# Optimization experiments

Measured on AMD Instinct MI355X. Metric: run time of the kernel, lower is better.

Reference implementation:

```python
import jax, jax.numpy as jnp
import numpy as np

B, T, C, H = 2, 2048, 1024, 16
D = C // H  # head_dim = 64

def setup_inputs() -> dict:
    key = jax.random.key(0)
    k0, k1, k2, k3, k4 = jax.random.split(key, 5)
    s = 1.0 / np.sqrt(C)
    return {
        "x": jax.random.normal(k0, (B, T, C), dtype=jnp.float32),
        "w_qkv": jax.random.uniform(k1, (C, 3 * C), jnp.float32, -s, s),
        "b_qkv": jax.random.uniform(k2, (3 * C,), jnp.float32, -s, s),
        "w_proj": jax.random.uniform(k3, (C, C), jnp.float32, -s, s),
        "b_proj": jax.random.uniform(k4, (C,), jnp.float32, -s, s),
    }

def reference(x, w_qkv, b_qkv, w_proj, b_proj):
    Bx, Tx, Cx = x.shape
    qkv = x @ w_qkv + b_qkv                      # [B,T,3C]
    q, k, v = jnp.split(qkv, 3, axis=-1)
    # [B,T,C] -> [B,H,T,D]
    def heads(t):
        return t.reshape(Bx, Tx, H, D).transpose(0, 2, 1, 3)
    q, k, v = heads(q), heads(k), heads(v)
    att = jnp.einsum('bhqd,bhkd->bhqk', q, k) / np.sqrt(D).astype(np.float32)
    causal = jnp.tril(jnp.ones((Tx, Tx), dtype=bool))
    att = jnp.where(causal, att, -jnp.inf)
    att = jax.nn.softmax(att, axis=-1)
    y = jnp.einsum('bhqk,bhkd->bhqd', att, v)    # [B,H,T,D]
    y = y.transpose(0, 2, 1, 3).reshape(Bx, Tx, Cx)
    return y @ w_proj + b_proj
```

## Files before the change

kernel.cpp:

```cpp
#include <hip/hip_runtime.h>

typedef short bf16x8 __attribute__((ext_vector_type(8)));
typedef float f32x4 __attribute__((ext_vector_type(4)));
typedef unsigned short u16;
typedef unsigned short u16x8 __attribute__((ext_vector_type(8)));
typedef unsigned short u16x4 __attribute__((ext_vector_type(4), may_alias));
typedef float f32x4_a __attribute__((ext_vector_type(4), may_alias));

__device__ __forceinline__ u16 f2bf(float f) {
    union { float f; unsigned u; } v; v.f = f;
    unsigned r = v.u + 0x7fffu + ((v.u >> 16) & 1u);
    return (u16)(r >> 16);
}
__device__ __forceinline__ u16 f2bf_rhu(float f) {
    union { float f; unsigned u; } v; v.f = f;
    return (u16)((v.u + 0x8000u) >> 16);
}

__device__ __forceinline__ void gld_lds16(const void* g, void* l) {
    __builtin_amdgcn_global_load_lds(
        (const __attribute__((address_space(1))) void*)g,
        (__attribute__((address_space(3))) void*)l, 16, 0, 0);
}

__global__ __launch_bounds__(256) void prep_kernel(
    const float* __restrict__ x, u16* __restrict__ xb,
    const float* __restrict__ w_qkv, u16* __restrict__ wqkvT,
    const float* __restrict__ w_proj, u16* __restrict__ wprojT) {
    __shared__ float tile[32][33];
    const int b = blockIdx.x, tid = threadIdx.x;
    if (b < 2048) {
        const int i = b * 256 + tid;
        float4 a = ((const float4*)x)[i * 2];
        float4 c = ((const float4*)x)[i * 2 + 1];
        u16x8 h;
        h[0] = f2bf(a.x); h[1] = f2bf(a.y); h[2] = f2bf(a.z); h[3] = f2bf(a.w);
        h[4] = f2bf(c.x); h[5] = f2bf(c.y); h[6] = f2bf(c.z); h[7] = f2bf(c.w);
        *(u16x8*)(xb + (size_t)i * 8) = h;
        return;
    }
    const float* in; u16* out; int N, bx;
    if (b < 5120) { bx = b - 2048; in = w_qkv; out = wqkvT; N = 3072; }
    else          { bx = b - 5120; in = w_proj; out = wprojT; N = 1024; }
    const int nblk = N / 32;
    const int n0 = (bx % nblk) * 32, k0 = (bx / nblk) * 32;
    const int tx = tid & 31, ty = tid >> 5;
#pragma unroll
    for (int i = 0; i < 32; i += 8)
        tile[ty + i][tx] = in[(size_t)(k0 + ty + i) * N + n0 + tx];
    __syncthreads();
#pragma unroll
    for (int i = 0; i < 32; i += 8)
        out[(size_t)(n0 + ty + i) * 1024 + k0 + tx] = f2bf(tile[tx][ty + i]);
}

#define QSCALE 0.180336880f

template <int OUTMODE, int BN>
__global__ __launch_bounds__(256) void gemm_m97(
    const u16* __restrict__ A, const u16* __restrict__ Bt,
    const float* __restrict__ bias, float* __restrict__ Cf,
    u16* __restrict__ Qo, u16* __restrict__ Ko, u16* __restrict__ Vt,
    int M, int N, int K) {
    constexpr int NF = BN / 32;
    __shared__ __align__(16) u16 lA[128 * 64];
    __shared__ __align__(16) u16 lB[BN * 64];

    const int tid = threadIdx.x;
    const int lane = tid & 63, wid = tid >> 6;
    const int wr = wid >> 1, wc = wid & 1;
    const int fr = lane & 15, fq = lane >> 4;
    const int m0 = blockIdx.y * 128, n0 = blockIdx.x * BN;

    const int gsrc = (lane & 7) ^ (lane >> 3);
    const u16* gA0 = A + (size_t)(m0 + (tid >> 3)) * K + gsrc * 8;
    const u16* gB0 = Bt + (size_t)(n0 + (tid >> 3)) * K + gsrc * 8;
    u16* lAw = lA + wid * 512;
    u16* lBw = lB + wid * 512;

    const int r7 = fr & 7;
    const int gk[2] = { ((0 + fq) ^ r7) * 8, ((4 + fq) ^ r7) * 8 };

    f32x4 acc[4][NF];
#pragma unroll
    for (int m = 0; m < 4; m++)
#pragma unroll
        for (int n = 0; n < NF; n++)
#pragma unroll
            for (int r = 0; r < 4; r++) acc[m][n][r] = 0.f;

    for (int k0 = 0; k0 < K; k0 += 64) {
        __syncthreads();
#pragma unroll
        for (int c = 0; c < 4; c++)
            gld_lds16(gA0 + (size_t)(c * 32) * K + k0, lAw + c * 2048);
#pragma unroll
        for (int c = 0; c < BN / 32; c++)
            gld_lds16(gB0 + (size_t)(c * 32) * K + k0, lBw + c * 2048);
        __syncthreads();

#pragma unroll
        for (int kf = 0; kf < 2; kf++) {
            bf16x8 a[4], b[NF];
#pragma unroll
            for (int m = 0; m < 4; m++)
                a[m] = *(const bf16x8*)&lA[(wr * 64 + m * 16 + fr) * 64 + gk[kf]];
#pragma unroll
            for (int n = 0; n < NF; n++)
                b[n] = *(const bf16x8*)&lB[(wc * (BN / 2) + n * 16 + fr) * 64 + gk[kf]];
#pragma unroll
            for (int m = 0; m < 4; m++)
#pragma unroll
                for (int n = 0; n < NF; n++)
                    acc[m][n] = __builtin_amdgcn_mfma_f32_16x16x32_bf16(a[m], b[n], acc[m][n], 0, 0, 0);
        }
    }

#pragma unroll
    for (int m = 0; m < 4; m++) {
#pragma unroll
        for (int n = 0; n < NF; n++) {
            const int row0 = m0 + wr * 64 + m * 16 + fq * 4;
            const int col = n0 + wc * (BN / 2) + n * 16 + fr;
            float v4[4];
#pragma unroll
            for (int r = 0; r < 4; r++) v4[r] = acc[m][n][r] + bias[col];
            if (OUTMODE == 0) {
                const int bb = row0 >> 11, t0 = row0 & 2047;
                const int sec = col >> 10, cc = col & 1023;
                const int h = cc >> 6, d = cc & 63;
                if (sec == 0) {
#pragma unroll
                    for (int r = 0; r < 4; r++)
                        Qo[(((size_t)(bb * 16 + h) * 2048 + t0 + r) << 6) + d] = f2bf(v4[r] * QSCALE);
                } else if (sec == 1) {
#pragma unroll
                    for (int r = 0; r < 4; r++)
                        Ko[(((size_t)(bb * 16 + h) * 2048 + t0 + r) << 6) + d] = f2bf(v4[r]);
                } else {
                    ushort4 p;
                    p.x = f2bf(v4[0]); p.y = f2bf(v4[1]); p.z = f2bf(v4[2]); p.w = f2bf(v4[3]);
                    *(ushort4*)&Vt[(((size_t)(bb * 16 + h) * 64 + d) << 11) + t0] = p;
                }
            } else {
#pragma unroll
                for (int r = 0; r < 4; r++)
                    Cf[(size_t)(row0 + r) * N + col] = v4[r];
            }
        }
    }
}

__global__ __launch_bounds__(256, 4) void attn_kernel(const u16* __restrict__ Q,
                                                      const u16* __restrict__ Kg,
                                                      const u16* __restrict__ Vt,
                                                      u16* __restrict__ O) {
    __shared__ __align__(16) u16 lK[2][64 * 64];
    __shared__ __align__(16) u16 lV[2][64 * 64];
    __shared__ __align__(16) u16 lP[4][32 * 32];

    const int tid = threadIdx.x;
    const int lane = tid & 63, wid = tid >> 6;
    const int fr = lane & 15, fq = lane >> 4;
    const int kw = wid >> 1, qw = wid & 1;
    const int bh = blockIdx.x & 31;
    const int qi = 31 - (blockIdx.x >> 5);
    const int qb0 = qi * 64;
    const size_t base = (size_t)bh * (2048 * 64);
    const u16* Qp = Q + base;
    const u16* Kp = Kg + base;
    const u16* Vp = Vt + base;

    const int q0w = qb0 + qw * 32;
    bf16x8 qa[2][2];
#pragma unroll
    for (int qg = 0; qg < 2; qg++)
#pragma unroll
        for (int kf = 0; kf < 2; kf++)
            qa[qg][kf] = *(const bf16x8*)&Qp[(size_t)(q0w + qg * 16 + fr) * 64 + kf * 32 + fq * 8];
    asm volatile("s_waitcnt vmcnt(0)" ::: "memory");

    bf16x8 vones;
#pragma unroll
    for (int j = 0; j < 8; j++) vones[j] = (short)0x3F80;

    f32x4 o[4][2], lsum[2];
#pragma unroll
    for (int qg = 0; qg < 2; qg++) {
#pragma unroll
        for (int r = 0; r < 4; r++) lsum[qg][r] = 0.f;
#pragma unroll
        for (int dg = 0; dg < 4; dg++)
#pragma unroll
            for (int r = 0; r < 4; r++) o[dg][qg][r] = 0.f;
    }

    const int srow0 = wid * 8 + (lane >> 3);
    const int gsrc = (lane & 7) ^ (lane >> 3);
    const u16* kSrc0 = Kp + (size_t)srow0 * 64 + gsrc * 8;
    const u16* vSrc0 = Vp + ((size_t)srow0 << 11) + gsrc * 8;

    const int r7 = fr & 7;
    const int gk0 = ((0 + fq) ^ r7) * 8;
    const int gk1 = ((4 + fq) ^ r7) * 8;
    const int gkv = ((kw * 4 + fq) ^ r7) * 8;

    const int nt = qi + 1;

#define STAGE(buf, kt0_)                                                        \
    do {                                                                        \
        const int _kt0 = (kt0_);                                                \
        u16* _lkw = &lK[buf][wid * 512];                                        \
        u16* _lvw = &lV[buf][wid * 512];                                        \
        gld_lds16(kSrc0 + (size_t)_kt0 * 64, _lkw);                             \
        gld_lds16(kSrc0 + (size_t)(_kt0 + 32) * 64, _lkw + 2048);               \
        gld_lds16(vSrc0 + _kt0, _lvw);                                          \
        gld_lds16(vSrc0 + ((size_t)32 << 11) + _kt0, _lvw + 2048);              \
    } while (0)

    STAGE(0, 0);

    for (int kt = 0; kt < nt; kt++) {
        const int cur = kt & 1;
        if (kt + 1 < nt) {
            STAGE(cur ^ 1, (kt + 1) << 6);
            asm volatile("s_waitcnt vmcnt(4)" ::: "memory");
        } else {
            asm volatile("s_waitcnt vmcnt(0)" ::: "memory");
        }
        __builtin_amdgcn_s_barrier();

        const int kt0 = kt << 6;
        const u16* lKc = lK[cur];
        const u16* lVc = lV[cur];

        f32x4 s[2][2];
#pragma unroll
        for (int kg = 0; kg < 2; kg++)
#pragma unroll
            for (int qg = 0; qg < 2; qg++)
#pragma unroll
                for (int r = 0; r < 4; r++) s[kg][qg][r] = 0.f;
        __builtin_amdgcn_s_setprio(1);
#pragma unroll
        for (int kg = 0; kg < 2; kg++) {
            const int krow = (kw * 32 + kg * 16 + fr) * 64;
            bf16x8 kb0 = *(const bf16x8*)&lKc[krow + gk0];
            bf16x8 kb1 = *(const bf16x8*)&lKc[krow + gk1];
#pragma unroll
            for (int qg = 0; qg < 2; qg++) {
                s[kg][qg] = __builtin_amdgcn_mfma_f32_16x16x32_bf16(kb0, qa[qg][0], s[kg][qg], 0, 0, 0);
                s[kg][qg] = __builtin_amdgcn_mfma_f32_16x16x32_bf16(kb1, qa[qg][1], s[kg][qg], 0, 0, 0);
            }
        }
        __builtin_amdgcn_s_setprio(0);

        if (kt == nt - 1) {
#pragma unroll
            for (int kg = 0; kg < 2; kg++) {
                const int kg0 = kt0 + kw * 32 + kg * 16 + fq * 4;
#pragma unroll
                for (int qg = 0; qg < 2; qg++) {
                    const int qg0 = q0w + qg * 16 + fr;
#pragma unroll
                    for (int r = 0; r < 4; r++)
                        if (kg0 + r > qg0) s[kg][qg][r] = -200.f;
                }
            }
        }

#pragma unroll
        for (int kg = 0; kg < 2; kg++)
#pragma unroll
            for (int qg = 0; qg < 2; qg++) {
                const int ql = qg * 16 + fr;
                u16x4 w;
                w[0] = f2bf_rhu(__builtin_amdgcn_exp2f(s[kg][qg][0]));
                w[1] = f2bf_rhu(__builtin_amdgcn_exp2f(s[kg][qg][1]));
                w[2] = f2bf_rhu(__builtin_amdgcn_exp2f(s[kg][qg][2]));
                w[3] = f2bf_rhu(__builtin_amdgcn_exp2f(s[kg][qg][3]));
                const int g = (kg * 2 + (fq >> 1)) ^ (ql & 3);
                *(u16x4*)&lP[wid][ql * 32 + g * 8 + (fq & 1) * 4] = w;
            }
        asm volatile("" ::: "memory");

        __builtin_amdgcn_s_setprio(1);
        bf16x8 va[4];
#pragma unroll
        for (int dg = 0; dg < 4; dg++)
            va[dg] = *(const bf16x8*)&lVc[(dg * 16 + fr) * 64 + gkv];
#pragma unroll
        for (int qg = 0; qg < 2; qg++) {
            const int ql = qg * 16 + fr;
            bf16x8 pb = *(const bf16x8*)&lP[wid][ql * 32 + (fq ^ (ql & 3)) * 8];
            lsum[qg] = __builtin_amdgcn_mfma_f32_16x16x32_bf16(vones, pb, lsum[qg], 0, 0, 0);
#pragma unroll
            for (int dg = 0; dg < 4; dg++)
                o[dg][qg] = __builtin_amdgcn_mfma_f32_16x16x32_bf16(va[dg], pb, o[dg][qg], 0, 0, 0);
        }
        __builtin_amdgcn_s_setprio(0);

        __builtin_amdgcn_s_barrier();
    }
#undef STAGE

    float* cmb = (float*)&lK[0][0];
    float* slab = cmb + (size_t)qw * 2560 + lane * 40;
    if (kw == 1) {
#pragma unroll
        for (int dg = 0; dg < 4; dg++)
#pragma unroll
            for (int qg = 0; qg < 2; qg++)
                *(f32x4_a*)&slab[(dg * 2 + qg) * 4] = o[dg][qg];
#pragma unroll
        for (int qg = 0; qg < 2; qg++)
            *(f32x4_a*)&slab[32 + qg * 4] = lsum[qg];
    }
    __syncthreads();
    if (kw == 0) {
#pragma unroll
        for (int dg = 0; dg < 4; dg++)
#pragma unroll
            for (int qg = 0; qg < 2; qg++) {
                f32x4_a p = *(const f32x4_a*)&slab[(dg * 2 + qg) * 4];
#pragma unroll
                for (int r = 0; r < 4; r++) o[dg][qg][r] += p[r];
            }
#pragma unroll
        for (int qg = 0; qg < 2; qg++) {
            f32x4_a p = *(const f32x4_a*)&slab[32 + qg * 4];
            lsum[qg][0] += p[0];
        }

        const int bb = bh >> 4, hh = bh & 15;
#pragma unroll
        for (int qg = 0; qg < 2; qg++) {
            const float inv = 1.f / lsum[qg][0];
            u16* orow = O + ((size_t)(bb * 2048 + q0w + qg * 16 + fr)) * 1024 + hh * 64 + fq * 4;
#pragma unroll
            for (int dg = 0; dg < 4; dg++) {
                ushort4 h;
                h.x = f2bf(o[dg][qg][0] * inv);
                h.y = f2bf(o[dg][qg][1] * inv);
                h.z = f2bf(o[dg][qg][2] * inv);
                h.w = f2bf(o[dg][qg][3] * inv);
                *(ushort4*)&orow[dg * 16] = h;
            }
        }
    }
}

extern "C" void kernel_launch(void* const* d_in, const int* in_sizes, int n_in,
                              void* d_out, int out_size, void* d_ws, size_t ws_size,
                              hipStream_t stream) {
    const float* x      = (const float*)d_in[0];
    const float* w_qkv  = (const float*)d_in[1];
    const float* b_qkv  = (const float*)d_in[2];
    const float* w_proj = (const float*)d_in[3];
    const float* b_proj = (const float*)d_in[4];
    float* out = (float*)d_out;

    u16* ws = (u16*)d_ws;
    u16* wqkvT  = ws;
    u16* wprojT = wqkvT + 3072 * 1024;
    u16* Qb     = wprojT + 1024 * 1024;
    u16* Kb     = Qb + 32 * 2048 * 64;
    u16* Vtb    = Kb + 32 * 2048 * 64;
    u16* xb     = Vtb + 32 * 2048 * 64;
    u16* attnO  = xb;

    prep_kernel<<<6144, 256, 0, stream>>>(x, xb, w_qkv, wqkvT, w_proj, wprojT);

    gemm_m97<0, 128><<<dim3(24, 32), 256, 0, stream>>>(
        xb, wqkvT, b_qkv, nullptr, Qb, Kb, Vtb, 4096, 3072, 1024);

    attn_kernel<<<1024, 256, 0, stream>>>(Qb, Kb, Vtb, attnO);

    gemm_m97<1, 64><<<dim3(16, 32), 256, 0, stream>>>(
        attnO, wprojT, b_proj, out, nullptr, nullptr, nullptr, 4096, 1024, 1024);
}
```

Measured before the change: 98.71 us.

## Load V fragments directly from global into registers, stage only K in LDS

V tiles are no longer staged through shared memory. Each wave reads its V MFMA operands straight from global (transposed Vt) into registers at the top of each iteration, and only K stays double-buffered in LDS via global_load_lds. This cuts LDS footprint and LDS traffic, which could raise occupancy. In exchange the V global loads sit on the critical path with little prefetch distance and less coalescing, and a full vmcnt(0) wait is now required before each barrier.

```diff
diff --git a/kernel.cpp b/kernel.cpp
--- a/kernel.cpp
+++ b/kernel.cpp
@@ -155,14 +155,16 @@
                                                       const u16* __restrict__ Kg,
                                                       const u16* __restrict__ Vt,
                                                       u16* __restrict__ O) {
-    __shared__ __align__(16) u16 lK[2][64 * 64];
-    __shared__ __align__(16) u16 lV[2][64 * 64];
-    __shared__ __align__(16) u16 lP[4][32 * 32];
+    __shared__ __align__(16) u16 smem[12288];
+    u16* lK0 = smem;
+    u16* lK1 = smem + 4096;
+    u16* lPw;
 
     const int tid = threadIdx.x;
     const int lane = tid & 63, wid = tid >> 6;
     const int fr = lane & 15, fq = lane >> 4;
     const int kw = wid >> 1, qw = wid & 1;
+    lPw = smem + 8192 + wid * 1024;
     const int bh = blockIdx.x & 31;
     const int qi = 31 - (blockIdx.x >> 5);
     const int qb0 = qi * 64;
@@ -198,41 +200,37 @@
     const int srow0 = wid * 8 + (lane >> 3);
     const int gsrc = (lane & 7) ^ (lane >> 3);
     const u16* kSrc0 = Kp + (size_t)srow0 * 64 + gsrc * 8;
-    const u16* vSrc0 = Vp + ((size_t)srow0 << 11) + gsrc * 8;
 
     const int r7 = fr & 7;
     const int gk0 = ((0 + fq) ^ r7) * 8;
     const int gk1 = ((4 + fq) ^ r7) * 8;
-    const int gkv = ((kw * 4 + fq) ^ r7) * 8;
+
+    const u16* vBase = Vp + (size_t)fr * 2048 + kw * 32 + fq * 8;
 
     const int nt = qi + 1;
 
-#define STAGE(buf, kt0_)                                                        \
+#define STAGE_K(bufp, kt0_)                                                     \
     do {                                                                        \
-        const int _kt0 = (kt0_);                                                \
-        u16* _lkw = &lK[buf][wid * 512];                                        \
-        u16* _lvw = &lV[buf][wid * 512];                                        \
-        gld_lds16(kSrc0 + (size_t)_kt0 * 64, _lkw);                             \
-        gld_lds16(kSrc0 + (size_t)(_kt0 + 32) * 64, _lkw + 2048);               \
-        gld_lds16(vSrc0 + _kt0, _lvw);                                          \
-        gld_lds16(vSrc0 + ((size_t)32 << 11) + _kt0, _lvw + 2048);              \
+        u16* _lkw = (bufp) + wid * 512;                                         \
+        gld_lds16(kSrc0 + (size_t)(kt0_) * 64, _lkw);                           \
+        gld_lds16(kSrc0 + (size_t)((kt0_) + 32) * 64, _lkw + 2048);             \
     } while (0)
 
-    STAGE(0, 0);
+    STAGE_K(lK0, 0);
+    asm volatile("s_waitcnt vmcnt(0)" ::: "memory");
+    __builtin_amdgcn_s_barrier();
 
     for (int kt = 0; kt < nt; kt++) {
-        const int cur = kt & 1;
-        if (kt + 1 < nt) {
-            STAGE(cur ^ 1, (kt + 1) << 6);
-            asm volatile("s_waitcnt vmcnt(4)" ::: "memory");
-        } else {
-            asm volatile("s_waitcnt vmcnt(0)" ::: "memory");
-        }
-        __builtin_amdgcn_s_barrier();
-
         const int kt0 = kt << 6;
-        const u16* lKc = lK[cur];
-        const u16* lVc = lV[cur];
+        const u16* lKc = (kt & 1) ? lK1 : lK0;
+        u16* lKn = (kt & 1) ? lK0 : lK1;
+
+        bf16x8 va[4];
+#pragma unroll
+        for (int dg = 0; dg < 4; dg++)
+            va[dg] = *(const bf16x8*)(vBase + (size_t)dg * 32768 + kt0);
+
+        if (kt + 1 < nt) STAGE_K(lKn, kt0 + 64);
 
         f32x4 s[2][2];
 #pragma unroll
@@ -280,19 +278,15 @@
                 w[2] = f2bf_rhu(__builtin_amdgcn_exp2f(s[kg][qg][2]));
                 w[3] = f2bf_rhu(__builtin_amdgcn_exp2f(s[kg][qg][3]));
                 const int g = (kg * 2 + (fq >> 1)) ^ (ql & 3);
-                *(u16x4*)&lP[wid][ql * 32 + g * 8 + (fq & 1) * 4] = w;
+                *(u16x4*)&lPw[ql * 32 + g * 8 + (fq & 1) * 4] = w;
             }
         asm volatile("" ::: "memory");
 
         __builtin_amdgcn_s_setprio(1);
-        bf16x8 va[4];
-#pragma unroll
-        for (int dg = 0; dg < 4; dg++)
-            va[dg] = *(const bf16x8*)&lVc[(dg * 16 + fr) * 64 + gkv];
 #pragma unroll
         for (int qg = 0; qg < 2; qg++) {
             const int ql = qg * 16 + fr;
-            bf16x8 pb = *(const bf16x8*)&lP[wid][ql * 32 + (fq ^ (ql & 3)) * 8];
+            bf16x8 pb = *(const bf16x8*)&lPw[ql * 32 + (fq ^ (ql & 3)) * 8];
             lsum[qg] = __builtin_amdgcn_mfma_f32_16x16x32_bf16(vones, pb, lsum[qg], 0, 0, 0);
 #pragma unroll
             for (int dg = 0; dg < 4; dg++)
@@ -300,11 +294,12 @@
         }
         __builtin_amdgcn_s_setprio(0);
 
+        if (kt + 1 < nt) asm volatile("s_waitcnt vmcnt(0)" ::: "memory");
         __builtin_amdgcn_s_barrier();
     }
-#undef STAGE
-
-    float* cmb = (float*)&lK[0][0];
+#undef STAGE_K
+
+    float* cmb = (float*)smem;
     float* slab = cmb + (size_t)qw * 2560 + lane * 40;
     if (kw == 1) {
 #pragma unroll
```

Result: slower. 113.6 us (+15.1%).
